# Kernel tuning notes

Measured on AMD Instinct MI355X. Metric: run time of the kernel, lower is better.

## Reference

```python
import jax, jax.numpy as jnp
import numpy as np
from jax.scipy.special import logsumexp

N, S, D, C = 64, 512, 768, 32


def setup_inputs() -> dict:
    key = jax.random.key(0)
    k1, k2, k3, k4, k5 = jax.random.split(key, 5)
    X = jax.random.normal(k1, (N, S, D), dtype=jnp.float32)
    W = jax.random.normal(k2, (D, C), dtype=jnp.float32) * 0.02
    T = jax.random.normal(k3, (C, C), dtype=jnp.float32) * 0.1
    # one-hot labels [N,S,C]
    lab_idx = jax.random.randint(k4, (N, S), 0, C)
    labels = jax.nn.one_hot(lab_idx, C, dtype=jnp.float32)
    # pad_mask: 1 for first `length` positions, 0 after (lengths in [S//2, S])
    lengths = jax.random.randint(k5, (N,), S // 2, S + 1)
    pad_mask = (jnp.arange(S)[None, :] < lengths[:, None]).astype(jnp.float32)
    return {"X": X, "W": W, "T": T, "labels": labels, "pad_mask": pad_mask}


def _crf_nll(X, W, T, labels, pad_mask):
    npots = jnp.einsum("nsd,dc->nsc", X, W)  # [N,S,C]
    m = pad_mask[..., None]                   # [N,S,1]

    # Faithful replication of the in-place masking loop:
    # prev starts as the ORIGINAL last timestep (t-1 == -1 at t=0 in torch).
    def prop(prev, xs):
        nt, mt = xs
        new = (1.0 - mt) * prev + mt * nt
        return new, new

    _, np_t = jax.lax.scan(
        prop, npots[:, -1, :],
        (jnp.swapaxes(npots, 0, 1), jnp.swapaxes(m, 0, 1)))
    npots = jnp.swapaxes(np_t, 0, 1)  # [N,S,C]

    # Backward messages: msgs[i,j] = lse_k(np[i+1,k] + T[j,k] + msgs[i+1,k]) * mask[i+1]
    def bwd(msg_next, xs):
        np_next, m_next = xs  # [N,C], [N,1]
        new = logsumexp(np_next[:, None, :] + T[None, :, :] + msg_next[:, None, :],
                        axis=-1) * m_next
        return new, new

    xs = (jnp.swapaxes(npots[:, 1:, :], 0, 1), jnp.swapaxes(m[:, 1:, :], 0, 1))
    init = jnp.zeros((npots.shape[0], npots.shape[2]), dtype=npots.dtype)
    _, msgs = jax.lax.scan(bwd, init, xs, reverse=True)
    bwd0 = msgs[0]  # message at position 0

    logZ = logsumexp(npots[:, 0, :] + bwd0, axis=-1)  # [N]

    # Unnormalized gold-path score
    score = jnp.sum(jnp.sum(npots * labels, axis=-1) * pad_mask, axis=-1)
    labels_idx = jnp.argmax(labels, axis=-1)          # [N,S]
    trans = T[labels_idx[:, :-1]]                     # [N,S-1,C]
    score = score + jnp.sum(
        jnp.sum(trans * labels[:, 1:, :], axis=-1) * pad_mask[:, 1:], axis=-1)

    return -jnp.mean(score - logZ)


def reference(X, W, T, labels, pad_mask):
    return _crf_nll(X, W, T, labels, pad_mask)
```

## Files before the change

### kernel.cpp

```cpp
#include <hip/hip_runtime.h>
#include <hip/hip_bf16.h>
#include <math.h>

#define N_ 64
#define S_ 512
#define D_ 768
#define C_ 32
#define KCH 16
#define LC 32
#define WT_LD 772
#define BS_LD 36
#define BS_PER (C_ * BS_LD)

typedef __attribute__((ext_vector_type(8))) short bf16x8;
typedef __attribute__((ext_vector_type(4))) float f32x4;
typedef __attribute__((ext_vector_type(16))) float f32x16;

__device__ inline ushort f2bf(float x) {
    unsigned int b = __builtin_bit_cast(unsigned int, x);
    return (ushort)((b + 0x7FFFu + ((b >> 16) & 1u)) >> 16);
}

__device__ inline unsigned cvt_pk_bf16(float lo, float hi) {
    unsigned r;
    asm("v_cvt_pk_bf16_f32 %0, %1, %2" : "=v"(r) : "v"(lo), "v"(hi));
    return r;
}

__global__ __launch_bounds__(512) void gemm_npots_mfma(const float* __restrict__ X,
                                                       const float* __restrict__ W,
                                                       float* __restrict__ npots,
                                                       float* __restrict__ accum,
                                                       unsigned* __restrict__ cnt_all) {
    __shared__ ushort WtS[C_ * WT_LD];
    const int tid = threadIdx.x;

    if (blockIdx.x == 0 && tid == 0) { accum[0] = 0.f; cnt_all[0] = 0u; }

    for (int i = tid; i < D_ * C_; i += 512) {
        const int k = i >> 5, c = i & 31;
        WtS[c * WT_LD + k] = f2bf(W[i]);
    }
    __syncthreads();

    const int w  = tid >> 6;
    const int l  = tid & 63;
    const int lr = l & 15;
    const int q  = l >> 4;
    const int m0 = blockIdx.x * 128 + w * 16;

    const float*  xrow = X + (size_t)(m0 + lr) * D_ + q * 8;
    const ushort* wb0  = &WtS[lr * WT_LD + q * 8];
    const ushort* wb1  = wb0 + 16 * WT_LD;

    f32x4  Aalo[2], Aahi[2], Balo[2], Bahi[2];
    f32x4 acc0 = {0.f, 0.f, 0.f, 0.f};
    f32x4 acc1 = {0.f, 0.f, 0.f, 0.f};

    #define LOADG(S, g)                                                      \
        {                                                                    \
            _Pragma("unroll")                                                \
            for (int j = 0; j < 2; ++j) {                                    \
                const int c_ = (g) * 2 + j;                                  \
                S##alo[j] = *(const f32x4*)(xrow + c_ * 32);                 \
                S##ahi[j] = *(const f32x4*)(xrow + c_ * 32 + 4);             \
            }                                                                \
        }

    #define COMPG(S, g)                                                      \
        {                                                                    \
            _Pragma("unroll")                                                \
            for (int j = 0; j < 2; ++j) {                                    \
                const int c_ = (g) * 2 + j;                                  \
                union { unsigned u[4]; bf16x8 v; } af;                       \
                af.u[0] = cvt_pk_bf16(S##alo[j][0], S##alo[j][1]);           \
                af.u[1] = cvt_pk_bf16(S##alo[j][2], S##alo[j][3]);           \
                af.u[2] = cvt_pk_bf16(S##ahi[j][0], S##ahi[j][1]);           \
                af.u[3] = cvt_pk_bf16(S##ahi[j][2], S##ahi[j][3]);           \
                const bf16x8 b0 = *(const bf16x8*)(wb0 + c_ * 32);           \
                const bf16x8 b1 = *(const bf16x8*)(wb1 + c_ * 32);           \
                acc0 = __builtin_amdgcn_mfma_f32_16x16x32_bf16(af.v, b0, acc0, 0, 0, 0); \
                acc1 = __builtin_amdgcn_mfma_f32_16x16x32_bf16(af.v, b1, acc1, 0, 0, 0); \
            }                                                                \
        }

    LOADG(A, 0);
    LOADG(B, 1);
    for (int g = 0; g < 6; ++g) {
        COMPG(A, 2 * g);
        if (g < 5) LOADG(A, 2 * g + 2);
        COMPG(B, 2 * g + 1);
        if (g < 5) LOADG(B, 2 * g + 3);
    }
    #undef LOADG
    #undef COMPG

    const int r0 = m0 + q * 4;
    #pragma unroll
    for (int reg = 0; reg < 4; ++reg) {
        npots[(size_t)(r0 + reg) * C_ + lr]      = acc0[reg];
        npots[(size_t)(r0 + reg) * C_ + lr + 16] = acc1[reg];
    }
}

__global__ __launch_bounds__(1024) void crf_scan(const float* __restrict__ npots,
                                                 const float* __restrict__ pad,
                                                 const float* __restrict__ T,
                                                 const float* __restrict__ labels,
                                                 float* __restrict__ accum,
                                                 unsigned* __restrict__ cnt_all,
                                                 float* __restrict__ out) {
    __shared__ float e_s[KCH * LC * C_];
    __shared__ float Bs[KCH * BS_PER];
    __shared__ float cls_s[KCH];
    __shared__ float sc_s[KCH];
    __shared__ __align__(16) float wcomb[32];

    const int n   = blockIdx.x;
    const int tid = threadIdx.x;
    const int w   = tid >> 6;
    const int l   = tid & 63;
    const int cc  = l & 31;
    const int h   = l >> 5;

    const float* pm = pad + (size_t)n * S_;
    float lsum = 0.f;
    for (int t = l; t < S_; t += 64) lsum += pm[t];
    #pragma unroll
    for (int o = 32; o >= 1; o >>= 1) lsum += __shfl_xor(lsum, o);
    const int len = (int)(lsum + 0.5f);

    {
        const int k  = w;
        const int lo = k * LC;
        const int hi = min(lo + LC, len - 1);
        float* Bout = &Bs[w * BS_PER];

        if (lo >= len - 1) {
            #pragma unroll
            for (int qq = 0; qq < 16; ++qq) {
                const int row = (qq & 3) + 8 * (qq >> 2) + 4 * h;
                Bout[row * BS_LD + cc] = (row == cc) ? 1.f : 0.f;
            }
            if (l == 0) cls_s[w] = 0.f;
        } else {
            const int cnt = hi - lo;
            float* ew = &e_s[w * (LC * C_)];
            const float* npn = npots + ((size_t)n * S_ + lo) * C_;
            for (int qd = l * 4; qd < cnt * C_; qd += 256) {
                const float4 v = *(const float4*)(npn + qd);
                *(float4*)&ew[qd] = make_float4(expf(v.x), expf(v.y), expf(v.z), expf(v.w));
            }
            asm volatile("s_waitcnt lgkmcnt(0)" ::: "memory");

            float glo[8], ghi[8];
            {
                const float* el = ew + (size_t)(cnt - 1) * C_;
                #pragma unroll
                for (int j = 0; j < 8; ++j) {
                    const int kk = 8 * h + j;
                    glo[j] = el[kk]      * expf(T[kk * C_ + cc]);
                    ghi[j] = el[kk + 16] * expf(T[(kk + 16) * C_ + cc]);
                }
            }

            if (cnt == 1) {
                #pragma unroll
                for (int j = 0; j < 8; ++j) {
                    Bout[(8 * h + j) * BS_LD + cc]      = glo[j];
                    Bout[(8 * h + j + 16) * BS_LD + cc] = ghi[j];
                }
                if (l == 0) cls_s[w] = 0.f;
            } else {
                union { unsigned u[4]; bf16x8 v; } ETalo, ETahi, blo, bhi;
                #pragma unroll
                for (int t = 0; t < 4; ++t) {
                    const int kk = 8 * h + 2 * t;
                    ETalo.u[t] = cvt_pk_bf16(expf(T[cc * C_ + kk]),      expf(T[cc * C_ + kk + 1]));
                    ETahi.u[t] = cvt_pk_bf16(expf(T[cc * C_ + kk + 16]), expf(T[cc * C_ + kk + 17]));
                    blo.u[t]   = cvt_pk_bf16(glo[2 * t], glo[2 * t + 1]);
                    bhi.u[t]   = cvt_pk_bf16(ghi[2 * t], ghi[2 * t + 1]);
                }

                float logscale = 0.f;
                int it = 0;
                for (int i = hi - 2; i >= lo; --i) {
                    f32x16 d = {};
                    d = __builtin_amdgcn_mfma_f32_32x32x16_bf16(ETalo.v, blo.v, d, 0, 0, 0);
                    d = __builtin_amdgcn_mfma_f32_32x32x16_bf16(ETahi.v, bhi.v, d, 0, 0, 0);

                    const float* ep = ew + (i - lo) * C_ + 4 * h;
                    const float4 e0 = *(const float4*)(ep);
                    const float4 e1 = *(const float4*)(ep + 8);
                    const float4 e2 = *(const float4*)(ep + 16);
                    const float4 e3 = *(const float4*)(ep + 24);
                    float sd[16];
                    sd[0]  = d[0]  * e0.x;  sd[1]  = d[1]  * e0.y;  sd[2]  = d[2]  * e0.z;  sd[3]  = d[3]  * e0.w;
                    sd[4]  = d[4]  * e1.x;  sd[5]  = d[5]  * e1.y;  sd[6]  = d[6]  * e1.z;  sd[7]  = d[7]  * e1.w;
                    sd[8]  = d[8]  * e2.x;  sd[9]  = d[9]  * e2.y;  sd[10] = d[10] * e2.z;  sd[11] = d[11] * e2.w;
                    sd[12] = d[12] * e3.x;  sd[13] = d[13] * e3.y;  sd[14] = d[14] * e3.z;  sd[15] = d[15] * e3.w;

                    if ((++it & 7) == 0) {
                        float m = sd[0];
                        #pragma unroll
                        for (int qq = 1; qq < 16; ++qq) m = fmaxf(m, sd[qq]);
                        #pragma unroll
                        for (int o = 32; o >= 1; o >>= 1) m = fmaxf(m, __shfl_xor(m, o));
                        logscale += logf(m);
                        const float inv = 1.f / m;
                        #pragma unroll
                        for (int qq = 0; qq < 16; ++qq) sd[qq] *= inv;
                    }

                    if (i > lo) {
                        const unsigned w0 = cvt_pk_bf16(sd[0],  sd[1]);
                        const unsigned w1 = cvt_pk_bf16(sd[2],  sd[3]);
                        const unsigned w2 = cvt_pk_bf16(sd[4],  sd[5]);
                        const unsigned w3 = cvt_pk_bf16(sd[6],  sd[7]);
                        const unsigned w4 = cvt_pk_bf16(sd[8],  sd[9]);
                        const unsigned w5 = cvt_pk_bf16(sd[10], sd[11]);
                        const unsigned w6 = cvt_pk_bf16(sd[12], sd[13]);
                        const unsigned w7 = cvt_pk_bf16(sd[14], sd[15]);
                        const unsigned x0 = (unsigned)__shfl_xor((int)w0, 32);
                        const unsigned x1 = (unsigned)__shfl_xor((int)w1, 32);
                        const unsigned x2 = (unsigned)__shfl_xor((int)w2, 32);
                        const unsigned x3 = (unsigned)__shfl_xor((int)w3, 32);
                        const unsigned x4 = (unsigned)__shfl_xor((int)w4, 32);
                        const unsigned x5 = (unsigned)__shfl_xor((int)w5, 32);
                        const unsigned x6 = (unsigned)__shfl_xor((int)w6, 32);
                        const unsigned x7 = (unsigned)__shfl_xor((int)w7, 32);
                        blo.u[0] = h ? x2 : w0;
                        blo.u[1] = h ? x3 : w1;
                        blo.u[2] = h ? w2 : x0;
                        blo.u[3] = h ? w3 : x1;
                        bhi.u[0] = h ? x6 : w4;
                        bhi.u[1] = h ? x7 : w5;
                        bhi.u[2] = h ? w6 : x4;
                        bhi.u[3] = h ? w7 : x5;
                    } else {
                        #pragma unroll
                        for (int qq = 0; qq < 16; ++qq)
                            Bout[((qq & 3) + 8 * (qq >> 2) + 4 * h) * BS_LD + cc] = sd[qq];
                    }
                }
                if (l == 0) cls_s[w] = logscale;
            }
        }
    }

    {
        const int tb = w * LC;
        int best = 0;
        if (l <= LC) {
            const int t = tb - 1 + l;
            if (t >= 0) {
                const float* lrow = labels + ((size_t)n * S_ + t) * C_;
                float bv = lrow[0];
                #pragma unroll
                for (int c = 1; c < C_; ++c) {
                    const float x = lrow[c];
                    if (x > bv) { bv = x; best = c; }
                }
            }
        }
        const int cur = __shfl(best, l + 1);
        float v = 0.f;
        if (l < LC) {
            const int t = tb + l;
            const float p = pad[(size_t)n * S_ + t];
            v = p * npots[((size_t)n * S_ + t) * C_ + cur];
            if (t >= 1) v = fmaf(p, T[best * C_ + cur], v);
        }
        #pragma unroll
        for (int o = 32; o >= 1; o >>= 1) v += __shfl_xor(v, o);
        if (l == 0) sc_s[w] = v;
    }

    __syncthreads();

    if (w == 0) {
        const int r  = l & 31;
        const int hh = l >> 5;

        float cls = (l < KCH) ? cls_s[l] : 0.f;
        #pragma unroll
        for (int o = 32; o >= 1; o >>= 1) cls += __shfl_xor(cls, o);

        float sc = (l < KCH) ? sc_s[l] : 0.f;
        #pragma unroll
        for (int o = 32; o >= 1; o >>= 1) sc += __shfl_xor(sc, o);

        const float np_last = npots[((size_t)n * S_ + (len - 1)) * C_ + r];
        float m0 = np_last;
        #pragma unroll
        for (int o = 32; o >= 1; o >>= 1) m0 = fmaxf(m0, __shfl_xor(m0, o));
        float logscale = m0 + cls;
        if (hh == 0) wcomb[r] = expf(np_last - m0);
        asm volatile("s_waitcnt lgkmcnt(0)" ::: "memory");

        float sn = 0.f;
        for (int k2 = KCH - 1; k2 >= 0; --k2) {
            float cb[16], wv2[16];
            const float* Brow = &Bs[k2 * BS_PER + r * BS_LD + hh * 16];
            #pragma unroll
            for (int t = 0; t < 4; ++t) *(float4*)&cb[t * 4] = *(const float4*)(Brow + t * 4);
            #pragma unroll
            for (int t = 0; t < 4; ++t) *(float4*)&wv2[t * 4] = *(const float4*)&wcomb[hh * 16 + t * 4];
            float s = 0.f;
            #pragma unroll
            for (int t = 0; t < 16; ++t) s = fmaf(cb[t], wv2[t], s);
            s += __shfl_xor(s, 32);

            float m = s;
            #pragma unroll
            for (int o = 16; o >= 1; o >>= 1) m = fmaxf(m, __shfl_xor(m, o));
            logscale += logf(m);
            sn = s / m;
            if (hh == 0) wcomb[r] = sn;
            asm volatile("s_waitcnt lgkmcnt(0)" ::: "memory");
        }
        float vz = (hh == 0) ? sn : 0.f;
        #pragma unroll
        for (int o = 32; o >= 1; o >>= 1) vz += __shfl_xor(vz, o);
        const float logZn = logf(vz) + logscale;

        if (l == 0) {
            atomicAdd(accum, sc - logZn);
            asm volatile("s_waitcnt vmcnt(0)" ::: "memory");
            const unsigned old = atomicAdd(cnt_all, 1u);
            if (old == (unsigned)(N_ - 1)) {
                const float total = atomicAdd(accum, 0.f);
                out[0] = -total / (float)N_;
            }
        }
    }
}

extern "C" void kernel_launch(void* const* d_in, const int* in_sizes, int n_in,
                              void* d_out, int out_size, void* d_ws, size_t ws_size,
                              hipStream_t stream) {
    const float* X      = (const float*)d_in[0];
    const float* W      = (const float*)d_in[1];
    const float* T      = (const float*)d_in[2];
    const float* labels = (const float*)d_in[3];
    const float* pad    = (const float*)d_in[4];
    float* out = (float*)d_out;

    float*    npots   = (float*)d_ws;
    float*    accum   = npots + (size_t)N_ * S_ * C_;
    unsigned* cnt_all = (unsigned*)(accum + 1);

    gemm_npots_mfma<<<(N_ * S_) / 128, 512, 0, stream>>>(X, W, npots, accum, cnt_all);
    crf_scan<<<N_, 1024, 0, stream>>>(npots, pad, T, labels, accum, cnt_all, out);
}
```

Baseline: 55.59 us.

## Split CRF scan into per-chunk kernel and separate combine kernel

The single 1024-thread-per-sequence scan kernel is split into a chunk_score kernel launched over (sequence, chunk), with one wave computing the chunk transfer matrix and another the gold-path score, plus a small combine_tail kernel that chains the chunk matrices. Chunk matrices, log-scales and partial scores now go through global workspace instead of LDS. The aim is to spread the 1024 chunk waves over more CUs instead of packing 16 waves into each of 64 blocks. The half-wave bf16 exchange also drops from eight shuffles to four by selecting before swapping. The cost is an extra kernel launch and global round-trips for the intermediate matrices.

```diff
diff --git a/kernel.cpp b/kernel.cpp
--- a/kernel.cpp
+++ b/kernel.cpp
@@ -9,8 +9,6 @@
 #define KCH 16
 #define LC 32
 #define WT_LD 772
-#define BS_LD 36
-#define BS_PER (C_ * BS_LD)
 
 typedef __attribute__((ext_vector_type(8))) short bf16x8;
 typedef __attribute__((ext_vector_type(4))) float f32x4;
@@ -103,153 +101,20 @@
     }
 }
 
-__global__ __launch_bounds__(1024) void crf_scan(const float* __restrict__ npots,
-                                                 const float* __restrict__ pad,
-                                                 const float* __restrict__ T,
-                                                 const float* __restrict__ labels,
-                                                 float* __restrict__ accum,
-                                                 unsigned* __restrict__ cnt_all,
-                                                 float* __restrict__ out) {
-    __shared__ float e_s[KCH * LC * C_];
-    __shared__ float Bs[KCH * BS_PER];
-    __shared__ float cls_s[KCH];
-    __shared__ float sc_s[KCH];
-    __shared__ __align__(16) float wcomb[32];
-
-    const int n   = blockIdx.x;
+__global__ __launch_bounds__(128) void chunk_score(const float* __restrict__ npots,
+                                                   const float* __restrict__ pad,
+                                                   const float* __restrict__ T,
+                                                   const float* __restrict__ labels,
+                                                   float* __restrict__ Bg,
+                                                   float* __restrict__ chunk_ls,
+                                                   float* __restrict__ scores_p) {
+    const int n = blockIdx.x, k = blockIdx.y;
     const int tid = threadIdx.x;
-    const int w   = tid >> 6;
-    const int l   = tid & 63;
-    const int cc  = l & 31;
-    const int h   = l >> 5;
-
-    const float* pm = pad + (size_t)n * S_;
-    float lsum = 0.f;
-    for (int t = l; t < S_; t += 64) lsum += pm[t];
-    #pragma unroll
-    for (int o = 32; o >= 1; o >>= 1) lsum += __shfl_xor(lsum, o);
-    const int len = (int)(lsum + 0.5f);
-
-    {
-        const int k  = w;
-        const int lo = k * LC;
-        const int hi = min(lo + LC, len - 1);
-        float* Bout = &Bs[w * BS_PER];
-
-        if (lo >= len - 1) {
-            #pragma unroll
-            for (int qq = 0; qq < 16; ++qq) {
-                const int row = (qq & 3) + 8 * (qq >> 2) + 4 * h;
-                Bout[row * BS_LD + cc] = (row == cc) ? 1.f : 0.f;
-            }
-            if (l == 0) cls_s[w] = 0.f;
-        } else {
-            const int cnt = hi - lo;
-            float* ew = &e_s[w * (LC * C_)];
-            const float* npn = npots + ((size_t)n * S_ + lo) * C_;
-            for (int qd = l * 4; qd < cnt * C_; qd += 256) {
-                const float4 v = *(const float4*)(npn + qd);
-                *(float4*)&ew[qd] = make_float4(expf(v.x), expf(v.y), expf(v.z), expf(v.w));
-            }
-            asm volatile("s_waitcnt lgkmcnt(0)" ::: "memory");
-
-            float glo[8], ghi[8];
-            {
-                const float* el = ew + (size_t)(cnt - 1) * C_;
-                #pragma unroll
-                for (int j = 0; j < 8; ++j) {
-                    const int kk = 8 * h + j;
-                    glo[j] = el[kk]      * expf(T[kk * C_ + cc]);
-                    ghi[j] = el[kk + 16] * expf(T[(kk + 16) * C_ + cc]);
-                }
-            }
-
-            if (cnt == 1) {
-                #pragma unroll
-                for (int j = 0; j < 8; ++j) {
-                    Bout[(8 * h + j) * BS_LD + cc]      = glo[j];
-                    Bout[(8 * h + j + 16) * BS_LD + cc] = ghi[j];
-                }
-                if (l == 0) cls_s[w] = 0.f;
-            } else {
-                union { unsigned u[4]; bf16x8 v; } ETalo, ETahi, blo, bhi;
-                #pragma unroll
-                for (int t = 0; t < 4; ++t) {
-                    const int kk = 8 * h + 2 * t;
-                    ETalo.u[t] = cvt_pk_bf16(expf(T[cc * C_ + kk]),      expf(T[cc * C_ + kk + 1]));
-                    ETahi.u[t] = cvt_pk_bf16(expf(T[cc * C_ + kk + 16]), expf(T[cc * C_ + kk + 17]));
-                    blo.u[t]   = cvt_pk_bf16(glo[2 * t], glo[2 * t + 1]);
-                    bhi.u[t]   = cvt_pk_bf16(ghi[2 * t], ghi[2 * t + 1]);
-                }
-
-                float logscale = 0.f;
-                int it = 0;
-                for (int i = hi - 2; i >= lo; --i) {
-                    f32x16 d = {};
-                    d = __builtin_amdgcn_mfma_f32_32x32x16_bf16(ETalo.v, blo.v, d, 0, 0, 0);
-                    d = __builtin_amdgcn_mfma_f32_32x32x16_bf16(ETahi.v, bhi.v, d, 0, 0, 0);
-
-                    const float* ep = ew + (i - lo) * C_ + 4 * h;
-                    const float4 e0 = *(const float4*)(ep);
-                    const float4 e1 = *(const float4*)(ep + 8);
-                    const float4 e2 = *(const float4*)(ep + 16);
-                    const float4 e3 = *(const float4*)(ep + 24);
-                    float sd[16];
-                    sd[0]  = d[0]  * e0.x;  sd[1]  = d[1]  * e0.y;  sd[2]  = d[2]  * e0.z;  sd[3]  = d[3]  * e0.w;
-                    sd[4]  = d[4]  * e1.x;  sd[5]  = d[5]  * e1.y;  sd[6]  = d[6]  * e1.z;  sd[7]  = d[7]  * e1.w;
-                    sd[8]  = d[8]  * e2.x;  sd[9]  = d[9]  * e2.y;  sd[10] = d[10] * e2.z;  sd[11] = d[11] * e2.w;
-                    sd[12] = d[12] * e3.x;  sd[13] = d[13] * e3.y;  sd[14] = d[14] * e3.z;  sd[15] = d[15] * e3.w;
-
-                    if ((++it & 7) == 0) {
-                        float m = sd[0];
-                        #pragma unroll
-                        for (int qq = 1; qq < 16; ++qq) m = fmaxf(m, sd[qq]);
-                        #pragma unroll
-                        for (int o = 32; o >= 1; o >>= 1) m = fmaxf(m, __shfl_xor(m, o));
-                        logscale += logf(m);
-                        const float inv = 1.f / m;
-                        #pragma unroll
-                        for (int qq = 0; qq < 16; ++qq) sd[qq] *= inv;
-                    }
-
-                    if (i > lo) {
-                        const unsigned w0 = cvt_pk_bf16(sd[0],  sd[1]);
-                        const unsigned w1 = cvt_pk_bf16(sd[2],  sd[3]);
-                        const unsigned w2 = cvt_pk_bf16(sd[4],  sd[5]);
-                        const unsigned w3 = cvt_pk_bf16(sd[6],  sd[7]);
-                        const unsigned w4 = cvt_pk_bf16(sd[8],  sd[9]);
-                        const unsigned w5 = cvt_pk_bf16(sd[10], sd[11]);
-                        const unsigned w6 = cvt_pk_bf16(sd[12], sd[13]);
-                        const unsigned w7 = cvt_pk_bf16(sd[14], sd[15]);
-                        const unsigned x0 = (unsigned)__shfl_xor((int)w0, 32);
-                        const unsigned x1 = (unsigned)__shfl_xor((int)w1, 32);
-                        const unsigned x2 = (unsigned)__shfl_xor((int)w2, 32);
-                        const unsigned x3 = (unsigned)__shfl_xor((int)w3, 32);
-                        const unsigned x4 = (unsigned)__shfl_xor((int)w4, 32);
-                        const unsigned x5 = (unsigned)__shfl_xor((int)w5, 32);
-                        const unsigned x6 = (unsigned)__shfl_xor((int)w6, 32);
-                        const unsigned x7 = (unsigned)__shfl_xor((int)w7, 32);
-                        blo.u[0] = h ? x2 : w0;
-                        blo.u[1] = h ? x3 : w1;
-                        blo.u[2] = h ? w2 : x0;
-                        blo.u[3] = h ? w3 : x1;
-                        bhi.u[0] = h ? x6 : w4;
-                        bhi.u[1] = h ? x7 : w5;
-                        bhi.u[2] = h ? w6 : x4;
-                        bhi.u[3] = h ? w7 : x5;
-                    } else {
-                        #pragma unroll
-                        for (int qq = 0; qq < 16; ++qq)
-                            Bout[((qq & 3) + 8 * (qq >> 2) + 4 * h) * BS_LD + cc] = sd[qq];
-                    }
-                }
-                if (l == 0) cls_s[w] = logscale;
-            }
-        }
-    }
-
-    {
-        const int tb = w * LC;
+    const int l = tid & 63;
+    __shared__ __align__(16) float e_lds[LC * C_];
+
+    if (tid >= 64) {
+        const int tb = k * LC;
         int best = 0;
         if (l <= LC) {
             const int t = tb - 1 + l;
@@ -273,65 +138,208 @@
         }
         #pragma unroll
         for (int o = 32; o >= 1; o >>= 1) v += __shfl_xor(v, o);
-        if (l == 0) sc_s[w] = v;
-    }
-
-    __syncthreads();
-
-    if (w == 0) {
-        const int r  = l & 31;
-        const int hh = l >> 5;
-
-        float cls = (l < KCH) ? cls_s[l] : 0.f;
-        #pragma unroll
-        for (int o = 32; o >= 1; o >>= 1) cls += __shfl_xor(cls, o);
-
-        float sc = (l < KCH) ? sc_s[l] : 0.f;
-        #pragma unroll
-        for (int o = 32; o >= 1; o >>= 1) sc += __shfl_xor(sc, o);
-
-        const float np_last = npots[((size_t)n * S_ + (len - 1)) * C_ + r];
-        float m0 = np_last;
-        #pragma unroll
-        for (int o = 32; o >= 1; o >>= 1) m0 = fmaxf(m0, __shfl_xor(m0, o));
-        float logscale = m0 + cls;
-        if (hh == 0) wcomb[r] = expf(np_last - m0);
+        if (l == 0) scores_p[n * KCH + k] = v;
+        return;
+    }
+
+    const int cc = l & 31;
+    const int h  = l >> 5;
+
+    const float* pm = pad + (size_t)n * S_;
+    float ls = 0.f;
+    for (int t = l; t < S_; t += 64) ls += pm[t];
+    #pragma unroll
+    for (int o = 32; o >= 1; o >>= 1) ls += __shfl_xor(ls, o);
+    const int len = (int)(ls + 0.5f);
+
+    float* Bout = Bg + ((size_t)n * KCH + k) * (C_ * C_);
+    const int lo = k * LC;
+    const int hi = min(lo + LC, len - 1);
+
+    if (lo >= len - 1) {
+        #pragma unroll
+        for (int qq = 0; qq < 16; ++qq) {
+            const int row = (qq & 3) + 8 * (qq >> 2) + 4 * h;
+            Bout[row * C_ + cc] = (row == cc) ? 1.f : 0.f;
+        }
+        if (l == 0) chunk_ls[n * KCH + k] = 0.f;
+        return;
+    }
+
+    const int cnt = hi - lo;
+
+    const float* npn = npots + ((size_t)n * S_ + lo) * C_;
+    for (int qd = l * 4; qd < cnt * C_; qd += 256) {
+        const float4 v = *(const float4*)(npn + qd);
+        *(float4*)&e_lds[qd] = make_float4(expf(v.x), expf(v.y), expf(v.z), expf(v.w));
+    }
+    asm volatile("s_waitcnt lgkmcnt(0)" ::: "memory");
+
+    float glo[8], ghi[8];
+    {
+        const float* el = e_lds + (size_t)(cnt - 1) * C_;
+        #pragma unroll
+        for (int j = 0; j < 8; ++j) {
+            const int kk = 8 * h + j;
+            glo[j] = el[kk]      * expf(T[kk * C_ + cc]);
+            ghi[j] = el[kk + 16] * expf(T[(kk + 16) * C_ + cc]);
+        }
+    }
+
+    if (cnt == 1) {
+        #pragma unroll
+        for (int j = 0; j < 8; ++j) {
+            Bout[(8 * h + j) * C_ + cc]      = glo[j];
+            Bout[(8 * h + j + 16) * C_ + cc] = ghi[j];
+        }
+        if (l == 0) chunk_ls[n * KCH + k] = 0.f;
+        return;
+    }
+
+    union { unsigned u[4]; bf16x8 v; } ETalo, ETahi, blo, bhi;
+    #pragma unroll
+    for (int t = 0; t < 4; ++t) {
+        const int kk = 8 * h + 2 * t;
+        ETalo.u[t] = cvt_pk_bf16(expf(T[cc * C_ + kk]),      expf(T[cc * C_ + kk + 1]));
+        ETahi.u[t] = cvt_pk_bf16(expf(T[cc * C_ + kk + 16]), expf(T[cc * C_ + kk + 17]));
+        blo.u[t]   = cvt_pk_bf16(glo[2 * t], glo[2 * t + 1]);
+        bhi.u[t]   = cvt_pk_bf16(ghi[2 * t], ghi[2 * t + 1]);
+    }
+
+    float logscale = 0.f;
+    int it = 0;
+    for (int i = hi - 2; i >= lo; --i) {
+        f32x16 d = {};
+        d = __builtin_amdgcn_mfma_f32_32x32x16_bf16(ETalo.v, blo.v, d, 0, 0, 0);
+        d = __builtin_amdgcn_mfma_f32_32x32x16_bf16(ETahi.v, bhi.v, d, 0, 0, 0);
+
+        const float* ep = e_lds + (i - lo) * C_ + 4 * h;
+        const float4 e0 = *(const float4*)(ep);
+        const float4 e1 = *(const float4*)(ep + 8);
+        const float4 e2 = *(const float4*)(ep + 16);
+        const float4 e3 = *(const float4*)(ep + 24);
+        float sd[16];
+        sd[0]  = d[0]  * e0.x;  sd[1]  = d[1]  * e0.y;  sd[2]  = d[2]  * e0.z;  sd[3]  = d[3]  * e0.w;
+        sd[4]  = d[4]  * e1.x;  sd[5]  = d[5]  * e1.y;  sd[6]  = d[6]  * e1.z;  sd[7]  = d[7]  * e1.w;
+        sd[8]  = d[8]  * e2.x;  sd[9]  = d[9]  * e2.y;  sd[10] = d[10] * e2.z;  sd[11] = d[11] * e2.w;
+        sd[12] = d[12] * e3.x;  sd[13] = d[13] * e3.y;  sd[14] = d[14] * e3.z;  sd[15] = d[15] * e3.w;
+
+        if ((++it & 7) == 0) {
+            float m = sd[0];
+            #pragma unroll
+            for (int qq = 1; qq < 16; ++qq) m = fmaxf(m, sd[qq]);
+            #pragma unroll
+            for (int o = 32; o >= 1; o >>= 1) m = fmaxf(m, __shfl_xor(m, o));
+            logscale += logf(m);
+            const float inv = 1.f / m;
+            #pragma unroll
+            for (int qq = 0; qq < 16; ++qq) sd[qq] *= inv;
+        }
+
+        if (i > lo) {
+            const unsigned w0 = cvt_pk_bf16(sd[0],  sd[1]);
+            const unsigned w1 = cvt_pk_bf16(sd[2],  sd[3]);
+            const unsigned w2 = cvt_pk_bf16(sd[4],  sd[5]);
+            const unsigned w3 = cvt_pk_bf16(sd[6],  sd[7]);
+            const unsigned w4 = cvt_pk_bf16(sd[8],  sd[9]);
+            const unsigned w5 = cvt_pk_bf16(sd[10], sd[11]);
+            const unsigned w6 = cvt_pk_bf16(sd[12], sd[13]);
+            const unsigned w7 = cvt_pk_bf16(sd[14], sd[15]);
+            const unsigned s0 = h ? w0 : w2;
+            const unsigned s1 = h ? w1 : w3;
+            const unsigned s2 = h ? w4 : w6;
+            const unsigned s3 = h ? w5 : w7;
+            const unsigned r0 = (unsigned)__shfl_xor((int)s0, 32);
+            const unsigned r1 = (unsigned)__shfl_xor((int)s1, 32);
+            const unsigned r2 = (unsigned)__shfl_xor((int)s2, 32);
+            const unsigned r3 = (unsigned)__shfl_xor((int)s3, 32);
+            blo.u[0] = h ? r0 : w0;
+            blo.u[1] = h ? r1 : w1;
+            blo.u[2] = h ? w2 : r0;
+            blo.u[3] = h ? w3 : r1;
+            bhi.u[0] = h ? r2 : w4;
+            bhi.u[1] = h ? r3 : w5;
+            bhi.u[2] = h ? w6 : r2;
+            bhi.u[3] = h ? w7 : r3;
+        } else {
+            #pragma unroll
+            for (int qq = 0; qq < 16; ++qq)
+                Bout[((qq & 3) + 8 * (qq >> 2) + 4 * h) * C_ + cc] = sd[qq];
+        }
+    }
+    if (l == 0) chunk_ls[n * KCH + k] = logscale;
+}
+
+__global__ __launch_bounds__(64) void combine_tail(const float* __restrict__ npots,
+                                                   const float* __restrict__ pad,
+                                                   const float* __restrict__ Bg,
+                                                   const float* __restrict__ chunk_ls,
+                                                   const float* __restrict__ scores_p,
+                                                   float* __restrict__ accum,
+                                                   unsigned* __restrict__ cnt_all,
+                                                   float* __restrict__ out) {
+    const int n = blockIdx.x;
+    const int l = threadIdx.x;
+    const int r = l & 31;
+    const int h = l >> 5;
+    __shared__ __align__(16) float wcomb[32];
+
+    const float* pm = pad + (size_t)n * S_;
+    float ls = 0.f;
+    for (int t = l; t < S_; t += 64) ls += pm[t];
+    #pragma unroll
+    for (int o = 32; o >= 1; o >>= 1) ls += __shfl_xor(ls, o);
+    const int len = (int)(ls + 0.5f);
+
+    float cls = (l < KCH) ? chunk_ls[n * KCH + l] : 0.f;
+    #pragma unroll
+    for (int o = 32; o >= 1; o >>= 1) cls += __shfl_xor(cls, o);
+
+    float sc = (l < KCH) ? scores_p[n * KCH + l] : 0.f;
+    #pragma unroll
+    for (int o = 32; o >= 1; o >>= 1) sc += __shfl_xor(sc, o);
+
+    const float np_last = npots[((size_t)n * S_ + (len - 1)) * C_ + r];
+    float m0 = np_last;
+    #pragma unroll
+    for (int o = 32; o >= 1; o >>= 1) m0 = fmaxf(m0, __shfl_xor(m0, o));
+    float logscale = m0 + cls;
+    if (h == 0) wcomb[r] = expf(np_last - m0);
+    asm volatile("s_waitcnt lgkmcnt(0)" ::: "memory");
+
+    float sn = 0.f;
+    for (int k2 = KCH - 1; k2 >= 0; --k2) {
+        float cb[16], wv2[16];
+        const float* Brow = Bg + ((size_t)n * KCH + k2) * (C_ * C_) + r * C_ + h * 16;
+        #pragma unroll
+        for (int t = 0; t < 4; ++t) *(float4*)&cb[t * 4] = *(const float4*)(Brow + t * 4);
+        #pragma unroll
+        for (int t = 0; t < 4; ++t) *(float4*)&wv2[t * 4] = *(const float4*)&wcomb[h * 16 + t * 4];
+        float s = 0.f;
+        #pragma unroll
+        for (int t = 0; t < 16; ++t) s = fmaf(cb[t], wv2[t], s);
+        s += __shfl_xor(s, 32);
+
+        float m = s;
+        #pragma unroll
+        for (int o = 16; o >= 1; o >>= 1) m = fmaxf(m, __shfl_xor(m, o));
+        logscale += logf(m);
+        sn = s / m;
+        if (h == 0) wcomb[r] = sn;
         asm volatile("s_waitcnt lgkmcnt(0)" ::: "memory");
-
-        float sn = 0.f;
-        for (int k2 = KCH - 1; k2 >= 0; --k2) {
-            float cb[16], wv2[16];
-            const float* Brow = &Bs[k2 * BS_PER + r * BS_LD + hh * 16];
-            #pragma unroll
-            for (int t = 0; t < 4; ++t) *(float4*)&cb[t * 4] = *(const float4*)(Brow + t * 4);
-            #pragma unroll
-            for (int t = 0; t < 4; ++t) *(float4*)&wv2[t * 4] = *(const float4*)&wcomb[hh * 16 + t * 4];
-            float s = 0.f;
-            #pragma unroll
-            for (int t = 0; t < 16; ++t) s = fmaf(cb[t], wv2[t], s);
-            s += __shfl_xor(s, 32);
-
-            float m = s;
-            #pragma unroll
-            for (int o = 16; o >= 1; o >>= 1) m = fmaxf(m, __shfl_xor(m, o));
-            logscale += logf(m);
-            sn = s / m;
-            if (hh == 0) wcomb[r] = sn;
-            asm volatile("s_waitcnt lgkmcnt(0)" ::: "memory");
-        }
-        float vz = (hh == 0) ? sn : 0.f;
-        #pragma unroll
-        for (int o = 32; o >= 1; o >>= 1) vz += __shfl_xor(vz, o);
-        const float logZn = logf(vz) + logscale;
-
-        if (l == 0) {
-            atomicAdd(accum, sc - logZn);
-            asm volatile("s_waitcnt vmcnt(0)" ::: "memory");
-            const unsigned old = atomicAdd(cnt_all, 1u);
-            if (old == (unsigned)(N_ - 1)) {
-                const float total = atomicAdd(accum, 0.f);
-                out[0] = -total / (float)N_;
-            }
+    }
+    float vz = (h == 0) ? sn : 0.f;
+    #pragma unroll
+    for (int o = 32; o >= 1; o >>= 1) vz += __shfl_xor(vz, o);
+    const float logZn = logf(vz) + logscale;
+
+    if (l == 0) {
+        atomicAdd(accum, sc - logZn);
+        asm volatile("s_waitcnt vmcnt(0)" ::: "memory");
+        const unsigned old = atomicAdd(cnt_all, 1u);
+        if (old == (unsigned)(N_ - 1)) {
+            const float total = atomicAdd(accum, 0.f);
+            out[0] = -total / (float)N_;
         }
     }
 }
@@ -346,10 +354,16 @@
     const float* pad    = (const float*)d_in[4];
     float* out = (float*)d_out;
 
-    float*    npots   = (float*)d_ws;
-    float*    accum   = npots + (size_t)N_ * S_ * C_;
-    unsigned* cnt_all = (unsigned*)(accum + 1);
+    float*    npots    = (float*)d_ws;
+    float*    Bg       = npots + (size_t)N_ * S_ * C_;
+    float*    chunk_ls = Bg + (size_t)N_ * KCH * C_ * C_;
+    float*    scores_p = chunk_ls + N_ * KCH;
+    float*    accum    = scores_p + N_ * KCH;
+    unsigned* cnt_all  = (unsigned*)(accum + 1);
 
     gemm_npots_mfma<<<(N_ * S_) / 128, 512, 0, stream>>>(X, W, npots, accum, cnt_all);
-    crf_scan<<<N_, 1024, 0, stream>>>(npots, pad, T, labels, accum, cnt_all, out);
-}
+    chunk_score<<<dim3(N_, KCH), 128, 0, stream>>>(npots, pad, T, labels, Bg,
+                                                   chunk_ls, scores_p);
+    combine_tail<<<N_, 64, 0, stream>>>(npots, pad, Bg, chunk_ls, scores_p,
+                                        accum, cnt_all, out);
+}
```

After: 54.74 us. No clear change (-1.5%).
